# Performance work log

Measured on AMD Instinct MI355X. Metric: run time of the kernel, lower is better.

Reference implementation:

```python
import jax, jax.numpy as jnp
import numpy as np

B, S, HID = 2, 2048, 1024
NH = 16
DK = HID // NH


def setup_inputs() -> dict:
    key0 = jax.random.key(0)
    ks = jax.random.split(key0, 16)
    inp = {
        "query": jax.random.normal(ks[0], (B, S, HID), dtype=jnp.float32),
        "key": jax.random.normal(ks[1], (B, S, HID), dtype=jnp.float32),
        "value": jax.random.normal(ks[2], (B, S, HID), dtype=jnp.float32),
        "bias": jax.random.uniform(ks[3], (B, S), dtype=jnp.float32),
        "mask": jax.random.randint(ks[4], (B, 1, S), 0, 2, dtype=jnp.int32),
        "wq": jax.random.normal(ks[5], (HID, HID), dtype=jnp.float32) * 0.02,
        "bq": jax.random.normal(ks[6], (HID,), dtype=jnp.float32) * 0.02,
        "wk": jax.random.normal(ks[7], (HID, HID), dtype=jnp.float32) * 0.02,
        "bk": jax.random.normal(ks[8], (HID,), dtype=jnp.float32) * 0.02,
        "wv": jax.random.normal(ks[9], (HID, HID), dtype=jnp.float32) * 0.02,
        "bv": jax.random.normal(ks[10], (HID,), dtype=jnp.float32) * 0.02,
        "wo": jax.random.normal(ks[11], (HID, HID), dtype=jnp.float32) * 0.02,
        "bo": jax.random.normal(ks[12], (HID,), dtype=jnp.float32) * 0.02,
    }
    return inp


def reference(query, key, value, bias, mask, wq, bq, wk, bk, wv, bv, wo, bo):
    b, s, hid = query.shape
    # attn_bias_type == 'both': gate K and V with per-token scalar bias
    # (dropout is eval-mode identity): x + p[..., None] * x
    key = key + bias[:, :, None] * key
    value = value + bias[:, :, None] * value

    def proj(x, w, bb):
        # torch Linear: x @ W.T + b, then split heads -> [b, nh, s, dk]
        y = x @ w.T + bb
        return y.reshape(b, s, NH, DK).transpose(0, 2, 1, 3)

    q = proj(query, wq, bq)
    k = proj(key, wk, bk)
    v = proj(value, wv, bv)

    scores = jnp.einsum("bhqd,bhkd->bhqk", q, k) / jnp.sqrt(jnp.asarray(DK, q.dtype))
    m = mask[:, None]  # [b,1,1,s] broadcast over heads and query positions
    scores = jnp.where(m == 0, jnp.asarray(-10000.0, scores.dtype), scores)
    p_attn = jax.nn.softmax(scores, axis=-1)
    x = jnp.einsum("bhqk,bhkd->bhqd", p_attn, v)
    x = x.transpose(0, 2, 1, 3).reshape(b, s, hid)
    return x @ wo.T + bo
```

## Files before the change

### kernel.cpp

```cpp
#include <hip/hip_runtime.h>
#include <stdint.h>

#define NB   2
#define SS   2048
#define HIDN 1024
#define NHEAD 16
#define DKK  64

typedef __attribute__((ext_vector_type(8))) short bf16x8;
typedef __attribute__((ext_vector_type(4))) float f32x4;

__device__ __forceinline__ uint16_t f2bf(float f) {
    uint32_t u = __float_as_uint(f);
    u += 0x7FFF + ((u >> 16) & 1);
    return (uint16_t)(u >> 16);
}
__device__ __forceinline__ uint32_t pk2(float f0, float f1) {
    uint32_t u0 = __float_as_uint(f0);
    uint32_t u1 = __float_as_uint(f1);
    u0 += 0x7FFF + ((u0 >> 16) & 1);
    u1 += 0x7FFF + ((u1 >> 16) & 1);
    return (u0 >> 16) | (u1 & 0xFFFF0000u);
}
__device__ __forceinline__ uint32_t cvtpk(float lo, float hi) {
    uint32_t r;
    asm("v_cvt_pk_bf16_f32 %0, %1, %2" : "=v"(r) : "v"(lo), "v"(hi));
    return r;
}
__device__ __forceinline__ float exp2_fast(float x) {
    float r;
    asm("v_exp_f32 %0, %1" : "=v"(r) : "v"(x));
    return r;
}
__device__ __forceinline__ uint4 pack8(const float* __restrict__ s, float sc) {
    float4 a = *(const float4*)s;
    float4 b = *(const float4*)(s + 4);
    uint4 r;
    r.x = pk2(sc * a.x, sc * a.y);
    r.y = pk2(sc * a.z, sc * a.w);
    r.z = pk2(sc * b.x, sc * b.y);
    r.w = pk2(sc * b.z, sc * b.w);
    return r;
}
__device__ __forceinline__ void gl_lds16(const uint16_t* g, uint16_t* l) {
    __builtin_amdgcn_global_load_lds((const __attribute__((address_space(1))) void*)g,
                                     (__attribute__((address_space(3))) void*)l,
                                     16, 0, 0);
}

__global__ __launch_bounds__(256, 4)
void cvt_all(const float* __restrict__ q, const float* __restrict__ k,
             const float* __restrict__ v, const float* __restrict__ bias,
             const float* __restrict__ w0, const float* __restrict__ w1,
             const float* __restrict__ w2, const float* __restrict__ w3,
             uint16_t* __restrict__ q16, uint16_t* __restrict__ k16,
             uint16_t* __restrict__ v16, uint16_t* __restrict__ w16o)
{
    int i = blockIdx.x * 256 + threadIdx.x;
    if (i < 524288) {
        size_t e = (size_t)i * 8;
        float sc = 1.0f + bias[i >> 7];
        *(uint4*)(q16 + e) = pack8(q + e, 1.0f);
        *(uint4*)(k16 + e) = pack8(k + e, sc);
        *(uint4*)(v16 + e) = pack8(v + e, sc);
    } else {
        int j = i - 524288;
        const float* src = (j < 131072) ? w0 : (j < 262144) ? w1
                         : (j < 393216) ? w2 : w3;
        size_t e = (size_t)(j & 131071) * 8;
        *(uint4*)(w16o + (size_t)(j >> 17) * 1048576 + e) = pack8(src + e, 1.0f);
    }
}

__device__ __forceinline__ void gemm_core(const uint16_t* __restrict__ A,
                                          const uint16_t* __restrict__ W,
                                          uint16_t* __restrict__ As,
                                          uint16_t* __restrict__ Bs,
                                          int m0, int n0,
                                          f32x4 acc[4][4])
{
    const int t    = threadIdx.x;
    const int w    = t >> 6;
    const int lane = t & 63;
    const int q    = lane >> 4;
    const int lr   = lane & 15;
    const int wr   = (w >> 1) * 64;
    const int wc   = (w & 1) * 64;
    const int srow = lane >> 3;
    const int sg   = (lane & 7) ^ srow;

    for (int it = 0; it < 16; ++it) {
        const int k0 = it * 64;
#pragma unroll
        for (int c = 0; c < 4; ++c) {
            int r = w * 32 + c * 8;
            gl_lds16(A + (size_t)(m0 + r + srow) * HIDN + k0 + sg * 8,
                     As + r * 64);
            gl_lds16(W + (size_t)(n0 + r + srow) * HIDN + k0 + sg * 8,
                     Bs + r * 64);
        }
        __syncthreads();

#pragma unroll
        for (int s = 0; s < 2; ++s) {
            bf16x8 af[4], bfr[4];
#pragma unroll
            for (int i = 0; i < 4; ++i)
                af[i] = *(const bf16x8*)&As[(wr + i * 16 + lr) * 64 +
                                            (((s * 4 + q) ^ (lr & 7)) * 8)];
#pragma unroll
            for (int j = 0; j < 4; ++j)
                bfr[j] = *(const bf16x8*)&Bs[(wc + j * 16 + lr) * 64 +
                                             (((s * 4 + q) ^ (lr & 7)) * 8)];
#pragma unroll
            for (int i = 0; i < 4; ++i)
#pragma unroll
                for (int j = 0; j < 4; ++j)
                    acc[i][j] = __builtin_amdgcn_mfma_f32_16x16x32_bf16(
                        af[i], bfr[j], acc[i][j], 0, 0, 0);
        }
        __syncthreads();
    }
}

__global__ __launch_bounds__(256, 3)
void gemm_qkv(const uint16_t* __restrict__ Qin, const uint16_t* __restrict__ Kin,
              const uint16_t* __restrict__ Vin, const uint16_t* __restrict__ W16,
              const float* __restrict__ bq, const float* __restrict__ bk,
              const float* __restrict__ bv,
              uint16_t* __restrict__ Qb, uint16_t* __restrict__ Kb,
              uint16_t* __restrict__ Vtb)
{
    __shared__ __align__(16) uint16_t Sh[2 * 128 * 64];
    uint16_t* As = Sh;
    uint16_t* Bs = Sh + 128 * 64;

    const int bid = (blockIdx.z << 8) | (blockIdx.y << 3) | blockIdx.x;
    const int swz = (bid & 7) * 96 + (bid >> 3);
    const int z   = swz >> 8;
    const int m0  = ((swz >> 3) & 31) * 128;
    const int n0  = (swz & 7) * 128;

    const uint16_t* A    = (z == 0) ? Qin : (z == 1) ? Kin : Vin;
    const uint16_t* W    = W16 + (size_t)z * 1048576;
    const float*    bias = (z == 0) ? bq : (z == 1) ? bk : bv;
    const float     osc  = (z == 0) ? 0.125f * 1.44269504f : 1.0f;

    const int t    = threadIdx.x;
    const int w    = t >> 6;
    const int lane = t & 63;
    const int q    = lane >> 4;
    const int lr   = lane & 15;
    const int wr   = (w >> 1) * 64;
    const int wc   = (w & 1) * 64;

    f32x4 acc[4][4] = {};
    gemm_core(A, W, As, Bs, m0, n0, acc);

    if (z < 2) {
        uint16_t* o = (z == 0) ? Qb : Kb;
#pragma unroll
        for (int i = 0; i < 4; ++i)
#pragma unroll
            for (int j = 0; j < 4; ++j) {
                int gn = n0 + wc + j * 16 + lr;
                float bvx = bias[gn];
#pragma unroll
                for (int r = 0; r < 4; ++r) {
                    int row = m0 + wr + i * 16 + q * 4 + r;
                    int b = row >> 11, s = row & 2047;
                    size_t dst = (size_t)b * (NHEAD * SS * DKK)
                               + (size_t)(gn >> 6) * (SS * DKK)
                               + (size_t)s * DKK + (gn & 63);
                    o[dst] = f2bf((acc[i][j][r] + bvx) * osc);
                }
            }
    } else {
        uint16_t* Tr = Sh;
        int b = m0 >> 11;
#pragma unroll
        for (int hh = 0; hh < 2; ++hh) {
            if ((w & 1) == hh) {
#pragma unroll
                for (int j = 0; j < 4; ++j) {
                    int dl = j * 16 + lr;
                    float bvx = bias[n0 + hh * 64 + dl];
#pragma unroll
                    for (int r = 0; r < 4; ++r) {
                        int sl = wr + (q * 4 + r);
                        Tr[dl * 136 + sl +  0] = f2bf(acc[0][j][r] + bvx);
                        Tr[dl * 136 + sl + 16] = f2bf(acc[1][j][r] + bvx);
                        Tr[dl * 136 + sl + 32] = f2bf(acc[2][j][r] + bvx);
                        Tr[dl * 136 + sl + 48] = f2bf(acc[3][j][r] + bvx);
                    }
                }
            }
            __syncthreads();
            int hgl = (n0 >> 6) + hh;
#pragma unroll
            for (int p = 0; p < 4; ++p) {
                int idx = p * 256 + t;
                int d   = idx >> 4;
                int sc8 = (idx & 15) * 8;
                size_t dst = ((size_t)(b * NHEAD + hgl) * DKK + d) * SS
                           + (m0 & 2047) + sc8;
                *(uint4*)&Vtb[dst] = *(const uint4*)&Tr[d * 136 + sc8];
            }
            __syncthreads();
        }
    }
}

__global__ __launch_bounds__(256, 3)
void gemm_out(const uint16_t* __restrict__ Xb, const uint16_t* __restrict__ W,
              const float* __restrict__ bias, float* __restrict__ out)
{
    __shared__ __align__(16) uint16_t Sh[2 * 128 * 64];
    uint16_t* As = Sh;
    uint16_t* Bs = Sh + 128 * 64;

    const int bid = (blockIdx.y << 3) | blockIdx.x;
    const int swz = (bid & 7) * 32 + (bid >> 3);
    const int m0  = (swz >> 3) * 128;
    const int n0  = (swz & 7) * 128;

    const int t    = threadIdx.x;
    const int w    = t >> 6;
    const int lane = t & 63;
    const int q    = lane >> 4;
    const int lr   = lane & 15;
    const int wr   = (w >> 1) * 64;
    const int wc   = (w & 1) * 64;

    f32x4 acc[4][4] = {};
    gemm_core(Xb, W, As, Bs, m0, n0, acc);

#pragma unroll
    for (int i = 0; i < 4; ++i)
#pragma unroll
        for (int j = 0; j < 4; ++j) {
            int gn = n0 + wc + j * 16 + lr;
            float bvx = bias[gn];
#pragma unroll
            for (int r = 0; r < 4; ++r) {
                int row = m0 + wr + i * 16 + q * 4 + r;
                out[(size_t)row * HIDN + gn] = acc[i][j][r] + bvx;
            }
        }
}

__global__ __launch_bounds__(512, 4)
void flash_attn(const uint16_t* __restrict__ Qg, const uint16_t* __restrict__ Kg,
                const uint16_t* __restrict__ Vtg, const int* __restrict__ mask,
                uint16_t* __restrict__ X)
{
    __shared__ __align__(16) uint16_t QP[128 * 64];
    __shared__ __align__(16) uint16_t Ks[64 * 64];
    __shared__ __align__(16) uint16_t Vs[64 * 64];
    __shared__ __align__(16) float Amf[SS];

    const int t    = threadIdx.x;
    const int w    = t >> 6;
    const int lane = t & 63;
    const int q    = lane >> 4;
    const int lr   = lane & 15;

    const int bid = (blockIdx.y << 4) | blockIdx.x;
    const int swz = (bid & 7) * 64 + (bid >> 3);
    const int bh  = swz >> 4;
    const int q0  = (swz & 15) * 128;

    const int b    = bh >> 4;
    const int h    = bh & 15;
    const size_t head = (size_t)bh * SS * DKK;

#pragma unroll
    for (int p = 0; p < 2; ++p) {
        int idx = p * 512 + t;
        int row = idx >> 3;
        int g   = idx & 7;
        *(uint4*)&QP[row * 64 + ((g ^ (row & 7)) * 8)] =
            *(const uint4*)(Qg + head + (size_t)(q0 + row) * DKK + g * 8);
    }
#pragma unroll
    for (int p = 0; p < 4; ++p) {
        int i = p * 512 + t;
        Amf[i] = (mask[b * SS + i] == 0) ? -14426.95f : 0.0f;
    }

    const int srow = t >> 3;
    const int sgf  = t & 7;
    const int scol = sgf * 8;
    const int swzc = (sgf ^ (srow & 7)) * 8;
    uint4 kreg = *(const uint4*)(Kg + head + (size_t)srow * DKK + scol);
    uint4 vreg = *(const uint4*)(Vtg + head + (size_t)srow * SS + scol);

    __syncthreads();

    bf16x8 qf[2];
#pragma unroll
    for (int s = 0; s < 2; ++s)
        qf[s] = *(const bf16x8*)&QP[(w * 16 + lr) * 64 +
                                    (((s * 4 + q) ^ (lr & 7)) * 8)];

    float mst = -1e30f, lst = 0.0f;
    f32x4 oacc[4] = {};

    for (int kv0 = 0; kv0 < SS; kv0 += 64) {
        *(uint4*)&Ks[srow * 64 + swzc] = kreg;
        *(uint4*)&Vs[srow * 64 + swzc] = vreg;
        __syncthreads();

        if (kv0 + 64 < SS) {
            kreg = *(const uint4*)(Kg + head + (size_t)(kv0 + 64 + srow) * DKK + scol);
            vreg = *(const uint4*)(Vtg + head + (size_t)srow * SS + kv0 + 64 + scol);
        }

        f32x4 st[4];
#pragma unroll
        for (int ni = 0; ni < 4; ++ni) {
            bf16x8 kf0 = *(const bf16x8*)&Ks[(ni * 16 + lr) * 64 +
                                             ((q ^ (lr & 7)) * 8)];
            bf16x8 kf1 = *(const bf16x8*)&Ks[(ni * 16 + lr) * 64 +
                                             (((4 + q) ^ (lr & 7)) * 8)];
            f32x4 z = {0.0f, 0.0f, 0.0f, 0.0f};
            z = __builtin_amdgcn_mfma_f32_16x16x32_bf16(kf0, qf[0], z, 0, 0, 0);
            z = __builtin_amdgcn_mfma_f32_16x16x32_bf16(kf1, qf[1], z, 0, 0, 0);
            st[ni] = z;
        }

        float rmax = -1e30f;
#pragma unroll
        for (int ni = 0; ni < 4; ++ni) {
            float4 am = *(const float4*)&Amf[kv0 + ni * 16 + q * 4];
            st[ni][0] += am.x; st[ni][1] += am.y;
            st[ni][2] += am.z; st[ni][3] += am.w;
#pragma unroll
            for (int r = 0; r < 4; ++r) rmax = fmaxf(rmax, st[ni][r]);
        }
        rmax = fmaxf(rmax, __shfl_xor(rmax, 16));
        rmax = fmaxf(rmax, __shfl_xor(rmax, 32));

        if (__any(rmax > mst + 11.5f)) {
            float mnew  = fmaxf(mst, rmax);
            float alpha = exp2_fast(mst - mnew);
            mst = mnew;
            lst *= alpha;
#pragma unroll
            for (int dj = 0; dj < 4; ++dj) {
                oacc[dj][0] *= alpha; oacc[dj][1] *= alpha;
                oacc[dj][2] *= alpha; oacc[dj][3] *= alpha;
            }
        }

        float rsum = 0.0f;
#pragma unroll
        for (int ni = 0; ni < 4; ++ni) {
            float p0 = exp2_fast(st[ni][0] - mst);
            float p1 = exp2_fast(st[ni][1] - mst);
            float p2 = exp2_fast(st[ni][2] - mst);
            float p3 = exp2_fast(st[ni][3] - mst);
            rsum += (p0 + p1) + (p2 + p3);
            uint2 pw = make_uint2(cvtpk(p0, p1), cvtpk(p2, p3));
            *(uint2*)&QP[(w * 16 + lr) * 64 +
                         (((ni * 2 + (q >> 1)) ^ (lr & 7)) * 8) + (q & 1) * 4] = pw;
        }
        lst += rsum;

#pragma unroll
        for (int ks = 0; ks < 2; ++ks) {
            bf16x8 pfB = *(const bf16x8*)&QP[(w * 16 + lr) * 64 +
                                             (((ks * 4 + q) ^ (lr & 7)) * 8)];
#pragma unroll
            for (int dj = 0; dj < 4; ++dj) {
                bf16x8 vfA = *(const bf16x8*)&Vs[(dj * 16 + lr) * 64 +
                                                 (((ks * 4 + q) ^ (lr & 7)) * 8)];
                oacc[dj] = __builtin_amdgcn_mfma_f32_16x16x32_bf16(vfA, pfB, oacc[dj], 0, 0, 0);
            }
        }
        __syncthreads();
    }

    {
        lst += __shfl_xor(lst, 16);
        lst += __shfl_xor(lst, 32);
        float inv = 1.0f / lst;
        int s = q0 + w * 16 + lr;
        uint16_t* xp = X + (size_t)(b * SS + s) * HIDN + h * DKK;
#pragma unroll
        for (int dj = 0; dj < 4; ++dj) {
            uint2 pw = make_uint2(cvtpk(oacc[dj][0] * inv, oacc[dj][1] * inv),
                                  cvtpk(oacc[dj][2] * inv, oacc[dj][3] * inv));
            *(uint2*)(xp + dj * 16 + q * 4) = pw;
        }
    }
}

extern "C" void kernel_launch(void* const* d_in, const int* in_sizes, int n_in,
                              void* d_out, int out_size, void* d_ws, size_t ws_size,
                              hipStream_t stream) {
    const float* query = (const float*)d_in[0];
    const float* key   = (const float*)d_in[1];
    const float* value = (const float*)d_in[2];
    const float* bias  = (const float*)d_in[3];
    const int*   mask  = (const int*)d_in[4];
    const float* wq = (const float*)d_in[5];
    const float* bq = (const float*)d_in[6];
    const float* wk = (const float*)d_in[7];
    const float* bk = (const float*)d_in[8];
    const float* wv = (const float*)d_in[9];
    const float* bv = (const float*)d_in[10];
    const float* wo = (const float*)d_in[11];
    const float* bo = (const float*)d_in[12];

    const size_t TEN = (size_t)NB * SS * HIDN;
    uint16_t* Qin = (uint16_t*)d_ws;
    uint16_t* Kin = Qin + TEN;
    uint16_t* Vin = Kin + TEN;
    uint16_t* W16 = Vin + TEN;
    uint16_t* Qb  = W16 + 4 * 1048576;
    uint16_t* Kb  = Qb + TEN;
    uint16_t* Vtb = Kb + TEN;
    uint16_t* Xb  = Qin;

    cvt_all<<<4096, 256, 0, stream>>>(query, key, value, bias,
                                      wq, wk, wv, wo, Qin, Kin, Vin, W16);
    gemm_qkv<<<dim3(8, 32, 3), 256, 0, stream>>>(Qin, Kin, Vin, W16,
                                                 bq, bk, bv, Qb, Kb, Vtb);
    flash_attn<<<dim3(SS / 128, NB * NHEAD), 512, 0, stream>>>(Qb, Kb, Vtb, mask, Xb);
    gemm_out<<<dim3(8, 32), 256, 0, stream>>>(Xb, W16 + 3 * 1048576, bo, (float*)d_out);
}
```

Before: 227.4 us.

## Fuse fp32-to-bf16 activation conversion into QKV GEMM A-tile loads

The separate pass that converted query/key/value to bf16 (with the per-token bias scaling) is removed. The QKV GEMM now reads fp32 activations directly, scales and packs them to bf16 in registers, and writes them swizzled into LDS, while weights are still converted by a smaller kernel. This saves a full write and re-read of three bf16 activation tensors, but the A-tile load becomes synchronous register traffic instead of direct global-to-LDS loads, and the GEMM re-reads fp32 A across 8 N tiles. Separately, s_setprio raises wave priority around the MFMA blocks in flash attention.

```diff
diff --git a/kernel.cpp b/kernel.cpp
--- a/kernel.cpp
+++ b/kernel.cpp
@@ -49,35 +49,24 @@
 }
 
 __global__ __launch_bounds__(256, 4)
-void cvt_all(const float* __restrict__ q, const float* __restrict__ k,
-             const float* __restrict__ v, const float* __restrict__ bias,
-             const float* __restrict__ w0, const float* __restrict__ w1,
-             const float* __restrict__ w2, const float* __restrict__ w3,
-             uint16_t* __restrict__ q16, uint16_t* __restrict__ k16,
-             uint16_t* __restrict__ v16, uint16_t* __restrict__ w16o)
-{
-    int i = blockIdx.x * 256 + threadIdx.x;
-    if (i < 524288) {
-        size_t e = (size_t)i * 8;
-        float sc = 1.0f + bias[i >> 7];
-        *(uint4*)(q16 + e) = pack8(q + e, 1.0f);
-        *(uint4*)(k16 + e) = pack8(k + e, sc);
-        *(uint4*)(v16 + e) = pack8(v + e, sc);
-    } else {
-        int j = i - 524288;
-        const float* src = (j < 131072) ? w0 : (j < 262144) ? w1
-                         : (j < 393216) ? w2 : w3;
-        size_t e = (size_t)(j & 131071) * 8;
-        *(uint4*)(w16o + (size_t)(j >> 17) * 1048576 + e) = pack8(src + e, 1.0f);
-    }
-}
-
-__device__ __forceinline__ void gemm_core(const uint16_t* __restrict__ A,
-                                          const uint16_t* __restrict__ W,
-                                          uint16_t* __restrict__ As,
-                                          uint16_t* __restrict__ Bs,
-                                          int m0, int n0,
-                                          f32x4 acc[4][4])
+void cvt_w(const float* __restrict__ w0, const float* __restrict__ w1,
+           const float* __restrict__ w2, const float* __restrict__ w3,
+           uint16_t* __restrict__ w16o)
+{
+    int j = blockIdx.x * 256 + threadIdx.x;
+    const float* src = (j < 131072) ? w0 : (j < 262144) ? w1
+                     : (j < 393216) ? w2 : w3;
+    size_t e = (size_t)(j & 131071) * 8;
+    *(uint4*)(w16o + (size_t)(j >> 17) * 1048576 + e) = pack8(src + e, 1.0f);
+}
+
+__device__ __forceinline__ void gemm_core_f32(const float* __restrict__ A,
+                                              const uint16_t* __restrict__ W,
+                                              const float* __restrict__ scv,
+                                              uint16_t* __restrict__ As,
+                                              uint16_t* __restrict__ Bs,
+                                              int m0, int n0,
+                                              f32x4 acc[4][4])
 {
     const int t    = threadIdx.x;
     const int w    = t >> 6;
@@ -89,15 +78,33 @@
     const int srow = lane >> 3;
     const int sg   = (lane & 7) ^ srow;
 
+    float scr[8];
+#pragma unroll
+    for (int c = 0; c < 8; ++c) {
+        int row = (c * 256 + t) >> 4;
+        scr[c] = scv ? (1.0f + scv[m0 + row]) : 1.0f;
+    }
+
     for (int it = 0; it < 16; ++it) {
         const int k0 = it * 64;
 #pragma unroll
         for (int c = 0; c < 4; ++c) {
             int r = w * 32 + c * 8;
-            gl_lds16(A + (size_t)(m0 + r + srow) * HIDN + k0 + sg * 8,
-                     As + r * 64);
             gl_lds16(W + (size_t)(n0 + r + srow) * HIDN + k0 + sg * 8,
                      Bs + r * 64);
+        }
+#pragma unroll
+        for (int c = 0; c < 8; ++c) {
+            int idx = c * 256 + t;
+            int row = idx >> 4;
+            int grp = idx & 15;
+            float4 a4 = *(const float4*)(A + (size_t)(m0 + row) * HIDN
+                                         + k0 + grp * 4);
+            float sc = scr[c];
+            uint2 pw = make_uint2(cvtpk(sc * a4.x, sc * a4.y),
+                                  cvtpk(sc * a4.z, sc * a4.w));
+            int g2 = (grp >> 1) ^ (row & 7);
+            *(uint2*)&As[row * 64 + g2 * 8 + (grp & 1) * 4] = pw;
         }
         __syncthreads();
 
@@ -123,29 +130,13 @@
     }
 }
 
-__global__ __launch_bounds__(256, 3)
-void gemm_qkv(const uint16_t* __restrict__ Qin, const uint16_t* __restrict__ Kin,
-              const uint16_t* __restrict__ Vin, const uint16_t* __restrict__ W16,
-              const float* __restrict__ bq, const float* __restrict__ bk,
-              const float* __restrict__ bv,
-              uint16_t* __restrict__ Qb, uint16_t* __restrict__ Kb,
-              uint16_t* __restrict__ Vtb)
-{
-    __shared__ __align__(16) uint16_t Sh[2 * 128 * 64];
-    uint16_t* As = Sh;
-    uint16_t* Bs = Sh + 128 * 64;
-
-    const int bid = (blockIdx.z << 8) | (blockIdx.y << 3) | blockIdx.x;
-    const int swz = (bid & 7) * 96 + (bid >> 3);
-    const int z   = swz >> 8;
-    const int m0  = ((swz >> 3) & 31) * 128;
-    const int n0  = (swz & 7) * 128;
-
-    const uint16_t* A    = (z == 0) ? Qin : (z == 1) ? Kin : Vin;
-    const uint16_t* W    = W16 + (size_t)z * 1048576;
-    const float*    bias = (z == 0) ? bq : (z == 1) ? bk : bv;
-    const float     osc  = (z == 0) ? 0.125f * 1.44269504f : 1.0f;
-
+__device__ __forceinline__ void gemm_core(const uint16_t* __restrict__ A,
+                                          const uint16_t* __restrict__ W,
+                                          uint16_t* __restrict__ As,
+                                          uint16_t* __restrict__ Bs,
+                                          int m0, int n0,
+                                          f32x4 acc[4][4])
+{
     const int t    = threadIdx.x;
     const int w    = t >> 6;
     const int lane = t & 63;
@@ -153,9 +144,78 @@
     const int lr   = lane & 15;
     const int wr   = (w >> 1) * 64;
     const int wc   = (w & 1) * 64;
+    const int srow = lane >> 3;
+    const int sg   = (lane & 7) ^ srow;
+
+    for (int it = 0; it < 16; ++it) {
+        const int k0 = it * 64;
+#pragma unroll
+        for (int c = 0; c < 4; ++c) {
+            int r = w * 32 + c * 8;
+            gl_lds16(A + (size_t)(m0 + r + srow) * HIDN + k0 + sg * 8,
+                     As + r * 64);
+            gl_lds16(W + (size_t)(n0 + r + srow) * HIDN + k0 + sg * 8,
+                     Bs + r * 64);
+        }
+        __syncthreads();
+
+#pragma unroll
+        for (int s = 0; s < 2; ++s) {
+            bf16x8 af[4], bfr[4];
+#pragma unroll
+            for (int i = 0; i < 4; ++i)
+                af[i] = *(const bf16x8*)&As[(wr + i * 16 + lr) * 64 +
+                                            (((s * 4 + q) ^ (lr & 7)) * 8)];
+#pragma unroll
+            for (int j = 0; j < 4; ++j)
+                bfr[j] = *(const bf16x8*)&Bs[(wc + j * 16 + lr) * 64 +
+                                             (((s * 4 + q) ^ (lr & 7)) * 8)];
+#pragma unroll
+            for (int i = 0; i < 4; ++i)
+#pragma unroll
+                for (int j = 0; j < 4; ++j)
+                    acc[i][j] = __builtin_amdgcn_mfma_f32_16x16x32_bf16(
+                        af[i], bfr[j], acc[i][j], 0, 0, 0);
+        }
+        __syncthreads();
+    }
+}
+
+__global__ __launch_bounds__(256, 3)
+void gemm_qkv(const float* __restrict__ Qf, const float* __restrict__ Kf,
+              const float* __restrict__ Vf, const float* __restrict__ binp,
+              const uint16_t* __restrict__ W16,
+              const float* __restrict__ bq, const float* __restrict__ bk,
+              const float* __restrict__ bv,
+              uint16_t* __restrict__ Qb, uint16_t* __restrict__ Kb,
+              uint16_t* __restrict__ Vtb)
+{
+    __shared__ __align__(16) uint16_t Sh[2 * 128 * 64];
+    uint16_t* As = Sh;
+    uint16_t* Bs = Sh + 128 * 64;
+
+    const int bid = (blockIdx.z << 8) | (blockIdx.y << 3) | blockIdx.x;
+    const int swz = (bid & 7) * 96 + (bid >> 3);
+    const int z   = swz >> 8;
+    const int m0  = ((swz >> 3) & 31) * 128;
+    const int n0  = (swz & 7) * 128;
+
+    const float*    A    = (z == 0) ? Qf : (z == 1) ? Kf : Vf;
+    const float*    scv  = (z == 0) ? nullptr : binp;
+    const uint16_t* W    = W16 + (size_t)z * 1048576;
+    const float*    bias = (z == 0) ? bq : (z == 1) ? bk : bv;
+    const float     osc  = (z == 0) ? 0.125f * 1.44269504f : 1.0f;
+
+    const int t    = threadIdx.x;
+    const int w    = t >> 6;
+    const int lane = t & 63;
+    const int q    = lane >> 4;
+    const int lr   = lane & 15;
+    const int wr   = (w >> 1) * 64;
+    const int wc   = (w & 1) * 64;
 
     f32x4 acc[4][4] = {};
-    gemm_core(A, W, As, Bs, m0, n0, acc);
+    gemm_core_f32(A, W, scv, As, Bs, m0, n0, acc);
 
     if (z < 2) {
         uint16_t* o = (z == 0) ? Qb : Kb;
@@ -317,6 +377,7 @@
         }
 
         f32x4 st[4];
+        __builtin_amdgcn_s_setprio(1);
 #pragma unroll
         for (int ni = 0; ni < 4; ++ni) {
             bf16x8 kf0 = *(const bf16x8*)&Ks[(ni * 16 + lr) * 64 +
@@ -328,6 +389,7 @@
             z = __builtin_amdgcn_mfma_f32_16x16x32_bf16(kf1, qf[1], z, 0, 0, 0);
             st[ni] = z;
         }
+        __builtin_amdgcn_s_setprio(0);
 
         float rmax = -1e30f;
 #pragma unroll
@@ -367,6 +429,7 @@
         }
         lst += rsum;
 
+        __builtin_amdgcn_s_setprio(1);
 #pragma unroll
         for (int ks = 0; ks < 2; ++ks) {
             bf16x8 pfB = *(const bf16x8*)&QP[(w * 16 + lr) * 64 +
@@ -378,6 +441,7 @@
                 oacc[dj] = __builtin_amdgcn_mfma_f32_16x16x32_bf16(vfA, pfB, oacc[dj], 0, 0, 0);
             }
         }
+        __builtin_amdgcn_s_setprio(0);
         __syncthreads();
     }
 
@@ -414,18 +478,14 @@
     const float* bo = (const float*)d_in[12];
 
     const size_t TEN = (size_t)NB * SS * HIDN;
-    uint16_t* Qin = (uint16_t*)d_ws;
-    uint16_t* Kin = Qin + TEN;
-    uint16_t* Vin = Kin + TEN;
-    uint16_t* W16 = Vin + TEN;
+    uint16_t* W16 = (uint16_t*)d_ws;
     uint16_t* Qb  = W16 + 4 * 1048576;
     uint16_t* Kb  = Qb + TEN;
     uint16_t* Vtb = Kb + TEN;
-    uint16_t* Xb  = Qin;
-
-    cvt_all<<<4096, 256, 0, stream>>>(query, key, value, bias,
-                                      wq, wk, wv, wo, Qin, Kin, Vin, W16);
-    gemm_qkv<<<dim3(8, 32, 3), 256, 0, stream>>>(Qin, Kin, Vin, W16,
+    uint16_t* Xb  = Vtb + TEN;
+
+    cvt_w<<<2048, 256, 0, stream>>>(wq, wk, wv, wo, W16);
+    gemm_qkv<<<dim3(8, 32, 3), 256, 0, stream>>>(query, key, value, bias, W16,
                                                  bq, bk, bv, Qb, Kb, Vtb);
     flash_attn<<<dim3(SS / 128, NB * NHEAD), 512, 0, stream>>>(Qb, Kb, Vtb, mask, Xb);
     gemm_out<<<dim3(8, 32), 256, 0, stream>>>(Xb, W16 + 3 * 1048576, bo, (float*)d_out);
```

Measured after the change: 233.9 us. +2.9%, slower.
